# Kernel optimization log

Hardware: AMD Instinct MI355X
Metric: run time of the kernel (lower is better)

Reference implementation:

```python
import jax, jax.numpy as jnp
import numpy as np

T, B, D = 256, 16, 512          # time, batch, intermediate_dim (GRU is seq-first)
HR = 256                         # router_dim
EXPERT_DIMS = [0, 128, 256, 512]
NUM_TASKS = 4
COST_EXP = 1.0
BN_EPS = 1e-5


def _gru(x, w_ih, w_hh, b_ih, b_hh):
    """PyTorch-semantics GRU over axis 0. x: (T, ..., D) -> (T, ..., H).
    Works batched (T,B,D) or unbatched (N,D) exactly like nn.GRU."""
    H = w_hh.shape[1]
    gi = x @ w_ih.T + b_ih            # (T, ..., 3H) input projections, done once
    h0 = jnp.zeros(x.shape[1:-1] + (H,), x.dtype)

    def step(h, gi_t):
        gh = h @ w_hh.T + b_hh
        i_r, i_z, i_n = jnp.split(gi_t, 3, axis=-1)
        h_r, h_z, h_n = jnp.split(gh, 3, axis=-1)
        r = jax.nn.sigmoid(i_r + h_r)
        z = jax.nn.sigmoid(i_z + h_z)
        n = jnp.tanh(i_n + r * h_n)
        h_new = (1.0 - z) * n + z * h
        return h_new, h_new

    _, ys = jax.lax.scan(step, h0, gi)
    return ys


def setup_inputs() -> dict:
    key = jax.random.key(0)
    ks = iter(jax.random.split(key, 64))

    def p(shape, fan_in):
        return (jax.random.normal(next(ks), shape, jnp.float32) / np.sqrt(fan_in)).astype(jnp.float32)

    inp = {
        'x': jax.random.normal(next(ks), (T, B, D), jnp.float32),
        'task_ids': jax.random.randint(next(ks), (T, B), 0, NUM_TASKS),
        # router params
        'router_w_ih': p((3 * HR, D), D),
        'router_w_hh': p((3 * HR, HR), HR),
        'router_b_ih': jnp.zeros((3 * HR,), jnp.float32),
        'router_b_hh': jnp.zeros((3 * HR,), jnp.float32),
        'router_out_w': p((len(EXPERT_DIMS), HR), HR),
        'router_out_b': jnp.zeros((len(EXPERT_DIMS),), jnp.float32),
    }
    for i, H in enumerate(EXPERT_DIMS):
        if H == 0:
            continue
        inp[f'e{i}_w_ih'] = p((3 * H, D), D)
        inp[f'e{i}_w_hh'] = p((3 * H, H), H)
        inp[f'e{i}_b_ih'] = jnp.zeros((3 * H,), jnp.float32)
        inp[f'e{i}_b_hh'] = jnp.zeros((3 * H,), jnp.float32)
        inp[f'e{i}_bn_g'] = jnp.ones((H,), jnp.float32)
        inp[f'e{i}_bn_b'] = jnp.zeros((H,), jnp.float32)
        inp[f'e{i}_out_w'] = p((D, H), H)
        inp[f'e{i}_out_b'] = jnp.zeros((D,), jnp.float32)
    return inp


def reference(x, task_ids,
              router_w_ih, router_w_hh, router_b_ih, router_b_hh,
              router_out_w, router_out_b,
              e1_w_ih, e1_w_hh, e1_b_ih, e1_b_hh, e1_bn_g, e1_bn_b, e1_out_w, e1_out_b,
              e2_w_ih, e2_w_hh, e2_b_ih, e2_b_hh, e2_bn_g, e2_bn_b, e2_out_w, e2_out_b,
              e3_w_ih, e3_w_hh, e3_b_ih, e3_b_hh, e3_bn_g, e3_bn_b, e3_out_w, e3_out_b):
    E = len(EXPERT_DIMS)
    # ---- router: GRU -> ReLU -> Linear -> softmax ----
    hs = _gru(x, router_w_ih, router_w_hh, router_b_ih, router_b_hh)   # (T,B,HR)
    logits = jax.nn.relu(hs) @ router_out_w.T + router_out_b           # (T,B,E)
    raw = jax.nn.softmax(logits, axis=-1)                              # raw_router_output
    # no dropout configured -> router_output == raw, all experts active

    # ---- task expert usage losses ----
    costs = jnp.asarray([d ** COST_EXP for d in EXPERT_DIMS], logits.dtype)
    eul = jnp.einsum('tbe,e->tb', raw, costs).reshape(-1)
    tflat = task_ids.reshape(-1)
    sums = jax.ops.segment_sum(eul, tflat, num_segments=NUM_TASKS)
    cnts = jax.ops.segment_sum(jnp.ones_like(eul), tflat, num_segments=NUM_TASKS)
    task_losses = sums / cnts                                           # (NUM_TASKS,)

    # ---- experts: each sees the flat (N,D) tokens as ONE unbatched GRU sequence ----
    flat_x = x.reshape(-1, D)                                           # (N,D)
    gates = raw.reshape(-1, E)                                          # (N,E)
    out = gates[:, 0:1] * flat_x                                        # expert 0 = identity

    eps = [(e1_w_ih, e1_w_hh, e1_b_ih, e1_b_hh, e1_bn_g, e1_bn_b, e1_out_w, e1_out_b),
           (e2_w_ih, e2_w_hh, e2_b_ih, e2_b_hh, e2_bn_g, e2_bn_b, e2_out_w, e2_out_b),
           (e3_w_ih, e3_w_hh, e3_b_ih, e3_b_hh, e3_bn_g, e3_bn_b, e3_out_w, e3_out_b)]
    for i, (w_ih, w_hh, b_ih, b_hh, g, b, ow, ob) in enumerate(eps, start=1):
        h = _gru(flat_x, w_ih, w_hh, b_ih, b_hh)                        # (N,H) unbatched seq
        mu = h.mean(0)
        var = ((h - mu) ** 2).mean(0)                                   # biased var (train-mode BN)
        hn = (h - mu) / jnp.sqrt(var + BN_EPS) * g + b
        eo = jax.nn.relu(hn) @ ow.T + ob                                # (N,D)
        out = out + gates[:, i:i + 1] * eo

    final_output = out.reshape(T, B, D)
    return final_output, raw, task_losses
```

## Files before the change

### kernel.cpp

```cpp
#include <hip/hip_runtime.h>
#include <math.h>

constexpr int TT = 256, BB = 16, DD = 512;
constexpr int NTOK = 4096;
constexpr int RTOT = 3456;
constexpr int E1OFF = 768, E2OFF = 1152, E3OFF = 1920;

constexpr size_t OFF_TSUM = 0;
constexpr size_t OFF_TCNT = 16;
constexpr size_t OFF_CNT  = 32;
constexpr size_t ZBYTES   = 64;
constexpr size_t OFF_GI   = 4096;
constexpr size_t OFF_HS   = OFF_GI  + (size_t)NTOK*RTOT*4;
constexpr size_t OFF_HA3  = OFF_HS  + (size_t)NTOK*256*4;
constexpr size_t OFF_HA2  = OFF_HA3 + (size_t)NTOK*512*4;
constexpr size_t OFF_HA1  = OFF_HA2 + (size_t)NTOK*256*4;
constexpr size_t OFF_AP   = OFF_HA1 + (size_t)NTOK*128*4;
constexpr size_t OFF_MU   = OFF_AP  + (size_t)NTOK*896*4;
constexpr size_t OFF_RSTD = OFF_MU  + 896*4;
constexpr size_t POISON_BYTES = (size_t)NTOK*(256+512+256+128)*4;

__device__ __forceinline__ bool is_poison(float v) {
  return __float_as_uint(v) == 0xAAAAAAAAu;
}

__device__ __forceinline__ float fast_sigmoid(float x) {
  const float xc = fminf(fmaxf(x, -30.f), 30.f);
  return __fdividef(1.f, 1.f + __expf(-xc));
}
__device__ __forceinline__ float fast_tanh(float x) {
  const float xc = fminf(fmaxf(x, -15.f), 15.f);
  const float e = __expf(-2.f * xc);
  return (1.f - e) * __fdividef(1.f, 1.f + e);
}

__global__ __launch_bounds__(256) void gemm1_kernel(
    const float* __restrict__ X,
    const float* __restrict__ wR, const float* __restrict__ w1,
    const float* __restrict__ w2, const float* __restrict__ w3,
    const float* __restrict__ bR, const float* __restrict__ b1,
    const float* __restrict__ b2, const float* __restrict__ b3,
    float* __restrict__ GI)
{
  __shared__ float At[32*64];
  __shared__ float Bt[32*64];
  const int n0 = blockIdx.x * 64;
  const int r0 = blockIdx.y * 64;
  const float* W; const float* bias; int rs;
  if (r0 < 768)       { W = wR; bias = bR; rs = 0; }
  else if (r0 < 1152) { W = w1; bias = b1; rs = 768; }
  else if (r0 < 1920) { W = w2; bias = b2; rs = 1152; }
  else                { W = w3; bias = b3; rs = 1920; }
  const int lr0 = r0 - rs;
  const int tid = threadIdx.x;
  const int lm = tid & 63, lk4 = tid >> 6;
  const int tx = tid & 15, ty = tid >> 4;
  float acc[4][4];
#pragma unroll
  for (int i = 0; i < 4; ++i)
#pragma unroll
    for (int q = 0; q < 4; ++q) acc[i][q] = 0.f;

  for (int kb = 0; kb < 512; kb += 32) {
    const float4 a0 = *(const float4*)(X + (size_t)(n0+lm)*512 + kb + lk4*8);
    const float4 a1 = *(const float4*)(X + (size_t)(n0+lm)*512 + kb + lk4*8 + 4);
    const float4 c0 = *(const float4*)(W + (size_t)(lr0+lm)*512 + kb + lk4*8);
    const float4 c1 = *(const float4*)(W + (size_t)(lr0+lm)*512 + kb + lk4*8 + 4);
    __syncthreads();
    At[(lk4*8+0)*64+lm]=a0.x; At[(lk4*8+1)*64+lm]=a0.y; At[(lk4*8+2)*64+lm]=a0.z; At[(lk4*8+3)*64+lm]=a0.w;
    At[(lk4*8+4)*64+lm]=a1.x; At[(lk4*8+5)*64+lm]=a1.y; At[(lk4*8+6)*64+lm]=a1.z; At[(lk4*8+7)*64+lm]=a1.w;
    Bt[(lk4*8+0)*64+lm]=c0.x; Bt[(lk4*8+1)*64+lm]=c0.y; Bt[(lk4*8+2)*64+lm]=c0.z; Bt[(lk4*8+3)*64+lm]=c0.w;
    Bt[(lk4*8+4)*64+lm]=c1.x; Bt[(lk4*8+5)*64+lm]=c1.y; Bt[(lk4*8+6)*64+lm]=c1.z; Bt[(lk4*8+7)*64+lm]=c1.w;
    __syncthreads();
#pragma unroll
    for (int k = 0; k < 32; ++k) {
      const float4 av = *(const float4*)&At[k*64 + ty*4];
      const float4 bv = *(const float4*)&Bt[k*64 + tx*4];
      acc[0][0]=fmaf(av.x,bv.x,acc[0][0]); acc[0][1]=fmaf(av.x,bv.y,acc[0][1]); acc[0][2]=fmaf(av.x,bv.z,acc[0][2]); acc[0][3]=fmaf(av.x,bv.w,acc[0][3]);
      acc[1][0]=fmaf(av.y,bv.x,acc[1][0]); acc[1][1]=fmaf(av.y,bv.y,acc[1][1]); acc[1][2]=fmaf(av.y,bv.z,acc[1][2]); acc[1][3]=fmaf(av.y,bv.w,acc[1][3]);
      acc[2][0]=fmaf(av.z,bv.x,acc[2][0]); acc[2][1]=fmaf(av.z,bv.y,acc[2][1]); acc[2][2]=fmaf(av.z,bv.z,acc[2][2]); acc[2][3]=fmaf(av.z,bv.w,acc[2][3]);
      acc[3][0]=fmaf(av.w,bv.x,acc[3][0]); acc[3][1]=fmaf(av.w,bv.y,acc[3][1]); acc[3][2]=fmaf(av.w,bv.z,acc[3][2]); acc[3][3]=fmaf(av.w,bv.w,acc[3][3]);
    }
  }
  const float4 bb = *(const float4*)(bias + lr0 + tx*4);
#pragma unroll
  for (int i = 0; i < 4; ++i) {
    float4 o;
    o.x = acc[i][0] + bb.x; o.y = acc[i][1] + bb.y; o.z = acc[i][2] + bb.z; o.w = acc[i][3] + bb.w;
    *(float4*)(GI + (size_t)(n0+ty*4+i)*RTOT + r0 + tx*4) = o;
  }
}

struct ScanArgs {
  const float* GI;
  const float* rwhh; const float* rbhh; float* hs;
  const float* w1; const float* b1; float* ha1;
  const float* w2; const float* b2; float* ha2;
  const float* w3; const float* b3; float* ha3;
  int* cnt;
};

template<int H, int OPW>
__device__ void expert_scan(const float* __restrict__ GIe, const float* __restrict__ whh,
                            const float* __restrict__ bhh, float* __restrict__ hall,
                            float* __restrict__ sm, int wg)
{
  constexpr int KCN = 512 / OPW;
  constexpr int CHUNK = H / KCN;
  constexpr int NF4 = CHUNK / 4;
  const int tid = threadIdx.x;
  const int j = tid / KCN, kc = tid % KCN;
  const int jg = wg * OPW + j;
  const int lane = tid & 63;

  float4 wr[NF4], wz[NF4], wn[NF4];
#pragma unroll
  for (int i4 = 0; i4 < NF4; ++i4) {
    const int kk = kc * CHUNK + ((i4 + kc) & (NF4 - 1)) * 4;
    wr[i4] = *(const float4*)(whh + (size_t)jg * H + kk);
    wz[i4] = *(const float4*)(whh + (size_t)(H + jg) * H + kk);
    wn[i4] = *(const float4*)(whh + (size_t)(2*H + jg) * H + kk);
  }
  float gbr = 0.f, gbz = 0.f, gbn = 0.f, hprev = 0.f;
  if (kc == 0) { gbr = bhh[jg]; gbz = bhh[H + jg]; gbn = bhh[2*H + jg]; }

  float gAr, gAz, gAn, gBr, gBz, gBn;
  { const float* g = GIe + (size_t)kc * RTOT;
    gAr = g[jg]; gAz = g[H + jg]; gAn = g[2*H + jg]; }
  { const float* g = GIe + (size_t)(KCN + kc) * RTOT;
    gBr = g[jg]; gBz = g[H + jg]; gBn = g[2*H + jg]; }

  for (int t = 0; t < NTOK; ++t) {
    float val = 0.f;
    if (tid < H && t > 0) {
      const volatile float* p = (const volatile float*)(hall + (size_t)(t - 1) * H + tid);
      val = *p;
      while (is_poison(val)) val = *p;
    }
    if (tid < H) sm[(size_t)(t & 1) * H + tid] = val;
    __syncthreads();
    const float* hbuf = sm + (size_t)(t & 1) * H;

    const int m = t & (KCN - 1);
    const int src = (lane & ~(KCN - 1)) | m;
    const float gr0 = __shfl(gAr, src);
    const float gz0 = __shfl(gAz, src);
    const float gn0 = __shfl(gAn, src);

    float pr = 0.f, pz = 0.f, pn = 0.f;
#pragma unroll
    for (int i4 = 0; i4 < NF4; ++i4) {
      const float4 h4 = *(const float4*)(hbuf + kc * CHUNK + ((i4 + kc) & (NF4 - 1)) * 4);
      pr = fmaf(wr[i4].x, h4.x, pr); pr = fmaf(wr[i4].y, h4.y, pr);
      pr = fmaf(wr[i4].z, h4.z, pr); pr = fmaf(wr[i4].w, h4.w, pr);
      pz = fmaf(wz[i4].x, h4.x, pz); pz = fmaf(wz[i4].y, h4.y, pz);
      pz = fmaf(wz[i4].z, h4.z, pz); pz = fmaf(wz[i4].w, h4.w, pz);
      pn = fmaf(wn[i4].x, h4.x, pn); pn = fmaf(wn[i4].y, h4.y, pn);
      pn = fmaf(wn[i4].z, h4.z, pn); pn = fmaf(wn[i4].w, h4.w, pn);
    }
#pragma unroll
    for (int off = KCN / 2; off; off >>= 1) {
      pr += __shfl_down(pr, off); pz += __shfl_down(pz, off); pn += __shfl_down(pn, off);
    }
    if (kc == 0) {
      const float rg = fast_sigmoid(gr0 + gbr + pr);
      const float zg = fast_sigmoid(gz0 + gbz + pz);
      const float nn = fast_tanh(gn0 + rg * (pn + gbn));
      const float hn = (1.f - zg) * nn + zg * hprev;
      hprev = hn;
      *(volatile float*)(hall + (size_t)t * H + jg) = hn;
    }
    if (m == KCN - 1) {
      gAr = gBr; gAz = gBz; gAn = gBn;
      const int nb = t + 1 + KCN;
      if (nb + kc < NTOK) {
        const float* g = GIe + (size_t)(nb + kc) * RTOT;
        gBr = g[jg]; gBz = g[H + jg]; gBn = g[2*H + jg];
      }
    }
  }
}

__device__ void router_scan(const float* __restrict__ GI, const float* __restrict__ whh,
                            const float* __restrict__ bhh, float* __restrict__ hs,
                            float* __restrict__ sm, int wg)
{
  float* hsmB = sm;
  float* pbuf = sm + 16 * 260;
  const int tid = threadIdx.x;
  const int j = tid >> 4, kc = tid & 15;
  const int jg = wg * 32 + j;
  float4 wr4[4], wz4[4], wn4[4];
#pragma unroll
  for (int i4 = 0; i4 < 4; ++i4) {
    const int kk = kc * 16 + ((i4 + kc) & 3) * 4;
    wr4[i4] = *(const float4*)(whh + (size_t)jg * 256 + kk);
    wz4[i4] = *(const float4*)(whh + (size_t)(256 + jg) * 256 + kk);
    wn4[i4] = *(const float4*)(whh + (size_t)(512 + jg) * 256 + kk);
  }
  const int b2 = tid >> 5, j2 = tid & 31;
  const int jg2 = wg * 32 + j2;
  const float gbr = bhh[jg2], gbz = bhh[256 + jg2], gbn = bhh[512 + jg2];
  float gr0, gz0, gn0, gr1, gz1, gn1;
  { const float* g = GI + (size_t)b2 * RTOT;        gr0 = g[jg2]; gz0 = g[256 + jg2]; gn0 = g[512 + jg2]; }
  { const float* g = GI + (size_t)(16 + b2) * RTOT; gr1 = g[jg2]; gz1 = g[256 + jg2]; gn1 = g[512 + jg2]; }
  const int pb = tid >> 5, pk = (tid & 31) * 8;

  for (int t = 0; t < TT; ++t) {
    float gr2 = 0.f, gz2 = 0.f, gn2 = 0.f;
    if (t + 2 < TT) {
      const float* g = GI + (size_t)((t + 2) * 16 + b2) * RTOT;
      gr2 = g[jg2]; gz2 = g[256 + jg2]; gn2 = g[512 + jg2];
    }
    float v[8];
    if (t == 0) {
#pragma unroll
      for (int u = 0; u < 8; ++u) v[u] = 0.f;
    } else {
      const volatile float* q = (const volatile float*)(hs + (size_t)(t - 1) * 4096 + tid * 8);
#pragma unroll
      for (int u = 0; u < 8; ++u) v[u] = q[u];
      bool bad = true;
      while (bad) {
        bad = false;
#pragma unroll
        for (int u = 0; u < 8; ++u)
          if (is_poison(v[u])) { v[u] = q[u]; bad = true; }
      }
    }
    __syncthreads();
    *(float4*)(hsmB + pb * 260 + pk)     = make_float4(v[0], v[1], v[2], v[3]);
    *(float4*)(hsmB + pb * 260 + pk + 4) = make_float4(v[4], v[5], v[6], v[7]);
    __syncthreads();
    float ar[16], az[16], an[16];
#pragma unroll
    for (int b = 0; b < 16; ++b) { ar[b] = 0.f; az[b] = 0.f; an[b] = 0.f; }
#pragma unroll
    for (int i4 = 0; i4 < 4; ++i4) {
      const int col = kc * 16 + ((i4 + kc) & 3) * 4;
#pragma unroll
      for (int b = 0; b < 16; ++b) {
        const float4 h4 = *(const float4*)(hsmB + b * 260 + col);
        ar[b] = fmaf(wr4[i4].x, h4.x, ar[b]); ar[b] = fmaf(wr4[i4].y, h4.y, ar[b]);
        ar[b] = fmaf(wr4[i4].z, h4.z, ar[b]); ar[b] = fmaf(wr4[i4].w, h4.w, ar[b]);
        az[b] = fmaf(wz4[i4].x, h4.x, az[b]); az[b] = fmaf(wz4[i4].y, h4.y, az[b]);
        az[b] = fmaf(wz4[i4].z, h4.z, az[b]); az[b] = fmaf(wz4[i4].w, h4.w, az[b]);
        an[b] = fmaf(wn4[i4].x, h4.x, an[b]); an[b] = fmaf(wn4[i4].y, h4.y, an[b]);
        an[b] = fmaf(wn4[i4].z, h4.z, an[b]); an[b] = fmaf(wn4[i4].w, h4.w, an[b]);
      }
    }
#pragma unroll
    for (int off = 8; off; off >>= 1) {
#pragma unroll
      for (int b = 0; b < 16; ++b) {
        ar[b] += __shfl_down(ar[b], off);
        az[b] += __shfl_down(az[b], off);
        an[b] += __shfl_down(an[b], off);
      }
    }
    if (kc == 0) {
#pragma unroll
      for (int b = 0; b < 16; ++b) {
        pbuf[(b * 32 + j) * 3 + 0] = ar[b];
        pbuf[(b * 32 + j) * 3 + 1] = az[b];
        pbuf[(b * 32 + j) * 3 + 2] = an[b];
      }
    }
    __syncthreads();
    const float pr = pbuf[(b2 * 32 + j2) * 3 + 0];
    const float pz = pbuf[(b2 * 32 + j2) * 3 + 1];
    const float pn = pbuf[(b2 * 32 + j2) * 3 + 2];
    const float hprev = hsmB[b2 * 260 + jg2];
    const float rg = 1.f / (1.f + expf(-(gr0 + gbr + pr)));
    const float zg = 1.f / (1.f + expf(-(gz0 + gbz + pz)));
    const float nn = tanhf(gn0 + rg * (pn + gbn));
    const float hn = (1.f - zg) * nn + zg * hprev;
    *(volatile float*)(hs + (size_t)t * 4096 + b2 * 256 + jg2) = hn;
    gr0 = gr1; gz0 = gz1; gn0 = gn1;
    gr1 = gr2; gz1 = gz2; gn1 = gn2;
  }
}

__global__ __launch_bounds__(512, 1) void scan_kernel(ScanArgs A)
{
  __shared__ __attribute__((aligned(16))) float sm[16 * 260 + 1536];
  __shared__ int role_s[2];
  if (threadIdx.x == 0) {
    unsigned x;
    asm volatile("s_getreg_b32 %0, hwreg(HW_REG_XCC_ID)" : "=s"(x));
    const int xcd = (int)(x & 7u);
    role_s[0] = xcd;
    role_s[1] = atomicAdd(A.cnt + xcd, 1);
  }
  __syncthreads();
  const int xcd = role_s[0], r = role_s[1];
  if (xcd == 0)      { if (r < 32) expert_scan<512, 16>(A.GI + E3OFF, A.w3, A.b3, A.ha3, sm, r); }
  else if (xcd == 1) { if (r < 8)  router_scan(A.GI, A.rwhh, A.rbhh, A.hs, sm, r); }
  else if (xcd == 2) { if (r < 8)  expert_scan<256, 32>(A.GI + E2OFF, A.w2, A.b2, A.ha2, sm, r); }
  else if (xcd == 3) { if (r < 4)  expert_scan<128, 32>(A.GI + E1OFF, A.w1, A.b1, A.ha1, sm, r); }
}

__global__ __launch_bounds__(256) void router_out_kernel(
    const float* __restrict__ hs, const float* __restrict__ ow, const float* __restrict__ ob,
    const int* __restrict__ tids, float* __restrict__ raw_out,
    float* __restrict__ tsum, float* __restrict__ tcnt)
{
  const int tid = threadIdx.x;
  const int lane = tid & 63, w = tid >> 6;
  const int n = blockIdx.x * 4 + w;
  float s0 = 0.f, s1 = 0.f, s2 = 0.f, s3 = 0.f;
#pragma unroll
  for (int q = 0; q < 4; ++q) {
    const int jj = lane + q * 64;
    float h = hs[(size_t)n * 256 + jj];
    h = h > 0.f ? h : 0.f;
    s0 = fmaf(h, ow[jj], s0);
    s1 = fmaf(h, ow[256 + jj], s1);
    s2 = fmaf(h, ow[512 + jj], s2);
    s3 = fmaf(h, ow[768 + jj], s3);
  }
  for (int off = 32; off; off >>= 1) {
    s0 += __shfl_xor(s0, off); s1 += __shfl_xor(s1, off);
    s2 += __shfl_xor(s2, off); s3 += __shfl_xor(s3, off);
  }
  if (lane == 0) {
    const float l0 = s0 + ob[0], l1 = s1 + ob[1], l2 = s2 + ob[2], l3 = s3 + ob[3];
    const float m = fmaxf(fmaxf(l0, l1), fmaxf(l2, l3));
    const float e0 = expf(l0 - m), e1 = expf(l1 - m), e2 = expf(l2 - m), e3 = expf(l3 - m);
    const float inv = 1.f / (e0 + e1 + e2 + e3);
    float4 rv; rv.x = e0 * inv; rv.y = e1 * inv; rv.z = e2 * inv; rv.w = e3 * inv;
    *(float4*)(raw_out + (size_t)n * 4) = rv;
    const float eul = rv.y * 128.f + rv.z * 256.f + rv.w * 512.f;
    const int tk = tids[n];
    atomicAdd(&tsum[tk], eul);
    atomicAdd(&tcnt[tk], 1.f);
  }
}

__global__ __launch_bounds__(256) void bn_stats_kernel(
    const float* __restrict__ h1, const float* __restrict__ h2, const float* __restrict__ h3,
    float* __restrict__ mu, float* __restrict__ rstd)
{
  const int c = blockIdx.x;
  const float* hp; int He, hc;
  if (c < 128)      { hp = h1; He = 128; hc = c; }
  else if (c < 384) { hp = h2; He = 256; hc = c - 128; }
  else              { hp = h3; He = 512; hc = c - 384; }
  float s = 0.f, s2 = 0.f;
  for (int r = threadIdx.x; r < NTOK; r += 256) {
    const float v = hp[(size_t)r * He + hc];
    s += v; s2 = fmaf(v, v, s2);
  }
  for (int off = 32; off; off >>= 1) { s += __shfl_xor(s, off); s2 += __shfl_xor(s2, off); }
  __shared__ float red[8];
  const int lane = threadIdx.x & 63, w = threadIdx.x >> 6;
  if (lane == 0) { red[w] = s; red[4 + w] = s2; }
  __syncthreads();
  if (threadIdx.x == 0) {
    const float S = red[0] + red[1] + red[2] + red[3];
    const float S2 = red[4] + red[5] + red[6] + red[7];
    const float m = S * (1.f / 4096.f);
    float v = S2 * (1.f / 4096.f) - m * m;
    v = v > 0.f ? v : 0.f;
    mu[c] = m;
    rstd[c] = 1.f / sqrtf(v + 1e-5f);
  }
}

__global__ __launch_bounds__(256) void aprime_kernel(
    const float* __restrict__ h1, const float* __restrict__ h2, const float* __restrict__ h3,
    const float* __restrict__ g1, const float* __restrict__ be1,
    const float* __restrict__ g2, const float* __restrict__ be2,
    const float* __restrict__ g3, const float* __restrict__ be3,
    const float* __restrict__ mu, const float* __restrict__ rstd,
    const float* __restrict__ raw, float* __restrict__ Ap,
    const float* __restrict__ tsum, const float* __restrict__ tcnt, float* __restrict__ tl_out)
{
  if (blockIdx.x == 4096) {
    if (threadIdx.x < 4) tl_out[threadIdx.x] = tsum[threadIdx.x] / tcnt[threadIdx.x];
    return;
  }
  const int n = blockIdx.x;
  for (int c = threadIdx.x; c < 896; c += 256) {
    const float* hp; const float* gg; const float* bb; int He, hc, e;
    if (c < 128)      { hp = h1; gg = g1; bb = be1; He = 128; hc = c;       e = 1; }
    else if (c < 384) { hp = h2; gg = g2; bb = be2; He = 256; hc = c - 128; e = 2; }
    else              { hp = h3; gg = g3; bb = be3; He = 512; hc = c - 384; e = 3; }
    const float h = hp[(size_t)n * He + hc];
    float v = (h - mu[c]) * rstd[c] * gg[hc] + bb[hc];
    v = v > 0.f ? v : 0.f;
    Ap[(size_t)n * 896 + c] = raw[(size_t)n * 4 + e] * v;
  }
}

__global__ __launch_bounds__(256) void out_gemm_kernel(
    const float* __restrict__ Ap,
    const float* __restrict__ ow1, const float* __restrict__ ow2, const float* __restrict__ ow3,
    const float* __restrict__ ob1, const float* __restrict__ ob2, const float* __restrict__ ob3,
    const float* __restrict__ X, const float* __restrict__ raw, float* __restrict__ out)
{
  __shared__ float At[32*64];
  __shared__ float Bt[32*64];
  const int n0 = blockIdx.x * 64;
  const int d0 = blockIdx.y * 64;
  const int tid = threadIdx.x;
  const int lm = tid & 63, lk4 = tid >> 6;
  const int tx = tid & 15, ty = tid >> 4;
  float acc[4][4];
#pragma unroll
  for (int i = 0; i < 4; ++i)
#pragma unroll
    for (int q = 0; q < 4; ++q) acc[i][q] = 0.f;

  for (int kb = 0; kb < 896; kb += 32) {
    const float* W; int He, ko;
    if (kb < 128)      { W = ow1; He = 128; ko = 0; }
    else if (kb < 384) { W = ow2; He = 256; ko = 128; }
    else               { W = ow3; He = 512; ko = 384; }
    const float4 a0 = *(const float4*)(Ap + (size_t)(n0+lm)*896 + kb + lk4*8);
    const float4 a1 = *(const float4*)(Ap + (size_t)(n0+lm)*896 + kb + lk4*8 + 4);
    const float4 c0 = *(const float4*)(W + (size_t)(d0+lm)*He + (kb - ko) + lk4*8);
    const float4 c1 = *(const float4*)(W + (size_t)(d0+lm)*He + (kb - ko) + lk4*8 + 4);
    __syncthreads();
    At[(lk4*8+0)*64+lm]=a0.x; At[(lk4*8+1)*64+lm]=a0.y; At[(lk4*8+2)*64+lm]=a0.z; At[(lk4*8+3)*64+lm]=a0.w;
    At[(lk4*8+4)*64+lm]=a1.x; At[(lk4*8+5)*64+lm]=a1.y; At[(lk4*8+6)*64+lm]=a1.z; At[(lk4*8+7)*64+lm]=a1.w;
    Bt[(lk4*8+0)*64+lm]=c0.x; Bt[(lk4*8+1)*64+lm]=c0.y; Bt[(lk4*8+2)*64+lm]=c0.z; Bt[(lk4*8+3)*64+lm]=c0.w;
    Bt[(lk4*8+4)*64+lm]=c1.x; Bt[(lk4*8+5)*64+lm]=c1.y; Bt[(lk4*8+6)*64+lm]=c1.z; Bt[(lk4*8+7)*64+lm]=c1.w;
    __syncthreads();
#pragma unroll
    for (int k = 0; k < 32; ++k) {
      const float4 av = *(const float4*)&At[k*64 + ty*4];
      const float4 bv = *(const float4*)&Bt[k*64 + tx*4];
      acc[0][0]=fmaf(av.x,bv.x,acc[0][0]); acc[0][1]=fmaf(av.x,bv.y,acc[0][1]); acc[0][2]=fmaf(av.x,bv.z,acc[0][2]); acc[0][3]=fmaf(av.x,bv.w,acc[0][3]);
      acc[1][0]=fmaf(av.y,bv.x,acc[1][0]); acc[1][1]=fmaf(av.y,bv.y,acc[1][1]); acc[1][2]=fmaf(av.y,bv.z,acc[1][2]); acc[1][3]=fmaf(av.y,bv.w,acc[1][3]);
      acc[2][0]=fmaf(av.z,bv.x,acc[2][0]); acc[2][1]=fmaf(av.z,bv.y,acc[2][1]); acc[2][2]=fmaf(av.z,bv.z,acc[2][2]); acc[2][3]=fmaf(av.z,bv.w,acc[2][3]);
      acc[3][0]=fmaf(av.w,bv.x,acc[3][0]); acc[3][1]=fmaf(av.w,bv.y,acc[3][1]); acc[3][2]=fmaf(av.w,bv.z,acc[3][2]); acc[3][3]=fmaf(av.w,bv.w,acc[3][3]);
    }
  }
#pragma unroll
  for (int i = 0; i < 4; ++i) {
    const int n = n0 + ty * 4 + i;
    const float4 g  = *(const float4*)(raw + (size_t)n * 4);
    const float4 xv = *(const float4*)(X + (size_t)n * 512 + d0 + tx * 4);
    const float4 o1 = *(const float4*)(ob1 + d0 + tx * 4);
    const float4 o2 = *(const float4*)(ob2 + d0 + tx * 4);
    const float4 o3 = *(const float4*)(ob3 + d0 + tx * 4);
    float4 o;
    o.x = acc[i][0] + g.x*xv.x + g.y*o1.x + g.z*o2.x + g.w*o3.x;
    o.y = acc[i][1] + g.x*xv.y + g.y*o1.y + g.z*o2.y + g.w*o3.y;
    o.z = acc[i][2] + g.x*xv.z + g.y*o1.z + g.z*o2.z + g.w*o3.z;
    o.w = acc[i][3] + g.x*xv.w + g.y*o1.w + g.z*o2.w + g.w*o3.w;
    *(float4*)(out + (size_t)n * 512 + d0 + tx * 4) = o;
  }
}

extern "C" void kernel_launch(void* const* d_in, const int* in_sizes, int n_in,
                              void* d_out, int out_size, void* d_ws, size_t ws_size,
                              hipStream_t stream) {
  const float* x    = (const float*)d_in[0];
  const int*   tids = (const int*)d_in[1];
  const float* rwih = (const float*)d_in[2];
  const float* rwhh = (const float*)d_in[3];
  const float* rbih = (const float*)d_in[4];
  const float* rbhh = (const float*)d_in[5];
  const float* row  = (const float*)d_in[6];
  const float* rob  = (const float*)d_in[7];
  const float* w1ih = (const float*)d_in[8];
  const float* w1hh = (const float*)d_in[9];
  const float* b1ih = (const float*)d_in[10];
  const float* b1hh = (const float*)d_in[11];
  const float* bn1g = (const float*)d_in[12];
  const float* bn1b = (const float*)d_in[13];
  const float* ow1  = (const float*)d_in[14];
  const float* ob1  = (const float*)d_in[15];
  const float* w2ih = (const float*)d_in[16];
  const float* w2hh = (const float*)d_in[17];
  const float* b2ih = (const float*)d_in[18];
  const float* b2hh = (const float*)d_in[19];
  const float* bn2g = (const float*)d_in[20];
  const float* bn2b = (const float*)d_in[21];
  const float* ow2  = (const float*)d_in[22];
  const float* ob2  = (const float*)d_in[23];
  const float* w3ih = (const float*)d_in[24];
  const float* w3hh = (const float*)d_in[25];
  const float* b3ih = (const float*)d_in[26];
  const float* b3hh = (const float*)d_in[27];
  const float* bn3g = (const float*)d_in[28];
  const float* bn3b = (const float*)d_in[29];
  const float* ow3  = (const float*)d_in[30];
  const float* ob3  = (const float*)d_in[31];

  char* ws = (char*)d_ws;
  float* tsum = (float*)(ws + OFF_TSUM);
  float* tcnt = (float*)(ws + OFF_TCNT);
  int*   cnt  = (int*)(ws + OFF_CNT);
  float* GI   = (float*)(ws + OFF_GI);
  float* hs   = (float*)(ws + OFF_HS);
  float* ha3  = (float*)(ws + OFF_HA3);
  float* ha2  = (float*)(ws + OFF_HA2);
  float* ha1  = (float*)(ws + OFF_HA1);
  float* Ap   = (float*)(ws + OFF_AP);
  float* mu   = (float*)(ws + OFF_MU);
  float* rstd = (float*)(ws + OFF_RSTD);

  float* outp = (float*)d_out;
  float* rawp = outp + (size_t)NTOK * DD;
  float* tlp  = rawp + (size_t)NTOK * 4;

  hipMemsetAsync(ws, 0, ZBYTES, stream);
  hipMemsetAsync(ws + OFF_HS, 0xAA, POISON_BYTES, stream);

  gemm1_kernel<<<dim3(64, 54), 256, 0, stream>>>(x, rwih, w1ih, w2ih, w3ih,
                                                 rbih, b1ih, b2ih, b3ih, GI);

  ScanArgs sa;
  sa.GI = GI; sa.rwhh = rwhh; sa.rbhh = rbhh; sa.hs = hs;
  sa.w1 = w1hh; sa.b1 = b1hh; sa.ha1 = ha1;
  sa.w2 = w2hh; sa.b2 = b2hh; sa.ha2 = ha2;
  sa.w3 = w3hh; sa.b3 = b3hh; sa.ha3 = ha3;
  sa.cnt = cnt;
  scan_kernel<<<dim3(320), dim3(512), 0, stream>>>(sa);

  router_out_kernel<<<dim3(1024), 256, 0, stream>>>(hs, row, rob, tids, rawp, tsum, tcnt);
  bn_stats_kernel<<<dim3(896), 256, 0, stream>>>(ha1, ha2, ha3, mu, rstd);
  aprime_kernel<<<dim3(4097), 256, 0, stream>>>(ha1, ha2, ha3, bn1g, bn1b, bn2g, bn2b,
                                                bn3g, bn3b, mu, rstd, rawp, Ap,
                                                tsum, tcnt, tlp);

  out_gemm_kernel<<<dim3(64, 8), 256, 0, stream>>>(Ap, ow1, ow2, ow3, ob1, ob2, ob3,
                                                   x, rawp, outp);
}
```

Before: 6.400 ms.

## Move expert-1 GRU scan to a single-block kernel and add cache-prefetch warps

The 128-wide expert-1 recurrence moves out of the multi-block polling scan into its own single 1024-thread block. There the hidden state is exchanged through shared memory with one barrier per step, instead of poison-polled global memory across four blocks. The combined scan kernel grows to 576 threads per block. The extra 64 threads in the expert scans touch hidden-state rows two steps ahead, to warm the cache for the polling loads. Because the new kernel is launched on the same stream before the combined scan, its 4096 serial steps no longer overlap with the other scans, which risks lengthening the critical path.

```diff
diff --git a/kernel.cpp b/kernel.cpp
--- a/kernel.cpp
+++ b/kernel.cpp
@@ -91,62 +91,61 @@
   }
 }
 
-struct ScanArgs {
-  const float* GI;
-  const float* rwhh; const float* rbhh; float* hs;
-  const float* w1; const float* b1; float* ha1;
-  const float* w2; const float* b2; float* ha2;
-  const float* w3; const float* b3; float* ha3;
-  int* cnt;
-};
-
-template<int H, int OPW>
-__device__ void expert_scan(const float* __restrict__ GIe, const float* __restrict__ whh,
-                            const float* __restrict__ bhh, float* __restrict__ hall,
-                            float* __restrict__ sm, int wg)
-{
-  constexpr int KCN = 512 / OPW;
-  constexpr int CHUNK = H / KCN;
-  constexpr int NF4 = CHUNK / 4;
+__global__ __launch_bounds__(1024, 1) void e1_scan_kernel(
+    const float* __restrict__ GIe, const float* __restrict__ whh,
+    const float* __restrict__ bhh, float* __restrict__ hall)
+{
+  constexpr int H = 128, CHUNK = 16, NF4 = 4;
+  __shared__ __attribute__((aligned(16))) float sm[2 * H];
   const int tid = threadIdx.x;
-  const int j = tid / KCN, kc = tid % KCN;
-  const int jg = wg * OPW + j;
   const int lane = tid & 63;
+  const int j = tid >> 3;
+  const int kc = tid & 7;
 
   float4 wr[NF4], wz[NF4], wn[NF4];
 #pragma unroll
   for (int i4 = 0; i4 < NF4; ++i4) {
     const int kk = kc * CHUNK + ((i4 + kc) & (NF4 - 1)) * 4;
-    wr[i4] = *(const float4*)(whh + (size_t)jg * H + kk);
-    wz[i4] = *(const float4*)(whh + (size_t)(H + jg) * H + kk);
-    wn[i4] = *(const float4*)(whh + (size_t)(2*H + jg) * H + kk);
+    wr[i4] = *(const float4*)(whh + (size_t)j * H + kk);
+    wz[i4] = *(const float4*)(whh + (size_t)(H + j) * H + kk);
+    wn[i4] = *(const float4*)(whh + (size_t)(2*H + j) * H + kk);
   }
   float gbr = 0.f, gbz = 0.f, gbn = 0.f, hprev = 0.f;
-  if (kc == 0) { gbr = bhh[jg]; gbz = bhh[H + jg]; gbn = bhh[2*H + jg]; }
-
-  float gAr, gAz, gAn, gBr, gBz, gBn;
-  { const float* g = GIe + (size_t)kc * RTOT;
-    gAr = g[jg]; gAz = g[H + jg]; gAn = g[2*H + jg]; }
-  { const float* g = GIe + (size_t)(KCN + kc) * RTOT;
-    gBr = g[jg]; gBz = g[H + jg]; gBn = g[2*H + jg]; }
+  if (kc == 0) { gbr = bhh[j]; gbz = bhh[H + j]; gbn = bhh[2*H + j]; }
+
+  float gA0r, gA0z, gA0n, gA1r, gA1z, gA1n;
+  float gB0r, gB0z, gB0n, gB1r, gB1z, gB1n;
+  { const float* g = GIe + (size_t)kc * RTOT;       gA0r=g[j]; gA0z=g[H+j]; gA0n=g[2*H+j]; }
+  { const float* g = GIe + (size_t)(8+kc) * RTOT;   gA1r=g[j]; gA1z=g[H+j]; gA1n=g[2*H+j]; }
+  { const float* g = GIe + (size_t)(16+kc) * RTOT;  gB0r=g[j]; gB0z=g[H+j]; gB0n=g[2*H+j]; }
+  { const float* g = GIe + (size_t)(24+kc) * RTOT;  gB1r=g[j]; gB1z=g[H+j]; gB1n=g[2*H+j]; }
+
+  if (tid < H) sm[tid] = 0.f;
+  __syncthreads();
 
   for (int t = 0; t < NTOK; ++t) {
-    float val = 0.f;
-    if (tid < H && t > 0) {
-      const volatile float* p = (const volatile float*)(hall + (size_t)(t - 1) * H + tid);
-      val = *p;
-      while (is_poison(val)) val = *p;
-    }
-    if (tid < H) sm[(size_t)(t & 1) * H + tid] = val;
-    __syncthreads();
+    if ((t & 15) == 0 && t > 0) {
+      gA0r=gB0r; gA0z=gB0z; gA0n=gB0n; gA1r=gB1r; gA1z=gB1z; gA1n=gB1n;
+      const int nb = t + 16;
+      if (nb + kc < NTOK) {
+        const float* g0 = GIe + (size_t)(nb + kc) * RTOT;
+        gB0r=g0[j]; gB0z=g0[H+j]; gB0n=g0[2*H+j];
+      }
+      if (nb + 8 + kc < NTOK) {
+        const float* g1 = GIe + (size_t)(nb + 8 + kc) * RTOT;
+        gB1r=g1[j]; gB1z=g1[H+j]; gB1n=g1[2*H+j];
+      }
+    }
+    const int hi = (t >> 3) & 1;
+    const float sr = hi ? gA1r : gA0r;
+    const float sz = hi ? gA1z : gA0z;
+    const float sn = hi ? gA1n : gA0n;
+    const int src = (lane & ~7) | (t & 7);
+    const float gr0 = __shfl(sr, src);
+    const float gz0 = __shfl(sz, src);
+    const float gn0 = __shfl(sn, src);
+
     const float* hbuf = sm + (size_t)(t & 1) * H;
-
-    const int m = t & (KCN - 1);
-    const int src = (lane & ~(KCN - 1)) | m;
-    const float gr0 = __shfl(gAr, src);
-    const float gz0 = __shfl(gAz, src);
-    const float gn0 = __shfl(gAn, src);
-
     float pr = 0.f, pz = 0.f, pn = 0.f;
 #pragma unroll
     for (int i4 = 0; i4 < NF4; ++i4) {
@@ -158,25 +157,124 @@
       pn = fmaf(wn[i4].x, h4.x, pn); pn = fmaf(wn[i4].y, h4.y, pn);
       pn = fmaf(wn[i4].z, h4.z, pn); pn = fmaf(wn[i4].w, h4.w, pn);
     }
-#pragma unroll
-    for (int off = KCN / 2; off; off >>= 1) {
-      pr += __shfl_down(pr, off); pz += __shfl_down(pz, off); pn += __shfl_down(pn, off);
-    }
+    pr += __shfl_down(pr, 4); pz += __shfl_down(pz, 4); pn += __shfl_down(pn, 4);
+    pr += __shfl_down(pr, 2); pz += __shfl_down(pz, 2); pn += __shfl_down(pn, 2);
+    pr += __shfl_down(pr, 1); pz += __shfl_down(pz, 1); pn += __shfl_down(pn, 1);
     if (kc == 0) {
       const float rg = fast_sigmoid(gr0 + gbr + pr);
       const float zg = fast_sigmoid(gz0 + gbz + pz);
       const float nn = fast_tanh(gn0 + rg * (pn + gbn));
       const float hn = (1.f - zg) * nn + zg * hprev;
       hprev = hn;
-      *(volatile float*)(hall + (size_t)t * H + jg) = hn;
-    }
-    if (m == KCN - 1) {
-      gAr = gBr; gAz = gBz; gAn = gBn;
-      const int nb = t + 1 + KCN;
-      if (nb + kc < NTOK) {
-        const float* g = GIe + (size_t)(nb + kc) * RTOT;
-        gBr = g[jg]; gBz = g[H + jg]; gBn = g[2*H + jg];
-      }
+      sm[(size_t)((t + 1) & 1) * H + j] = hn;
+      hall[(size_t)t * H + j] = hn;
+    }
+    __syncthreads();
+  }
+}
+
+struct ScanArgs {
+  const float* GI;
+  const float* rwhh; const float* rbhh; float* hs;
+  const float* w2; const float* b2; float* ha2;
+  const float* w3; const float* b3; float* ha3;
+  int* cnt;
+};
+
+template<int H, int OPW>
+__device__ void expert_scan(const float* __restrict__ GIe, const float* __restrict__ whh,
+                            const float* __restrict__ bhh, float* __restrict__ hall,
+                            float* __restrict__ sm, int wg)
+{
+  constexpr int KCN = 512 / OPW;
+  constexpr int CHUNK = H / KCN;
+  constexpr int NF4 = CHUNK / 4;
+  constexpr int PSTR = H / 64;
+  const int tid = threadIdx.x;
+  const bool act = (tid < 512);
+  const int lane = tid & 63;
+  const int j = (tid / KCN) & (OPW - 1);
+  const int kc = tid & (KCN - 1);
+  const int jg = wg * OPW + j;
+
+  float4 wr[NF4], wz[NF4], wn[NF4];
+  float gbr = 0.f, gbz = 0.f, gbn = 0.f, hprev = 0.f;
+  float gAr = 0.f, gAz = 0.f, gAn = 0.f, gBr = 0.f, gBz = 0.f, gBn = 0.f;
+  if (act) {
+#pragma unroll
+    for (int i4 = 0; i4 < NF4; ++i4) {
+      const int kk = kc * CHUNK + ((i4 + kc) & (NF4 - 1)) * 4;
+      wr[i4] = *(const float4*)(whh + (size_t)jg * H + kk);
+      wz[i4] = *(const float4*)(whh + (size_t)(H + jg) * H + kk);
+      wn[i4] = *(const float4*)(whh + (size_t)(2*H + jg) * H + kk);
+    }
+    if (kc == 0) { gbr = bhh[jg]; gbz = bhh[H + jg]; gbn = bhh[2*H + jg]; }
+    { const float* g = GIe + (size_t)kc * RTOT;
+      gAr = g[jg]; gAz = g[H + jg]; gAn = g[2*H + jg]; }
+    { const float* g = GIe + (size_t)(KCN + kc) * RTOT;
+      gBr = g[jg]; gBz = g[H + jg]; gBn = g[2*H + jg]; }
+  } else {
+    const int l = tid - 512;
+    volatile const float* p0 = (volatile const float*)(hall + (size_t)0 * H + l * PSTR);
+    volatile const float* p1 = (volatile const float*)(hall + (size_t)1 * H + l * PSTR);
+    float d0 = *p0, d1 = *p1;
+    asm volatile("" :: "v"(d0), "v"(d1));
+  }
+
+  for (int t = 0; t < NTOK; ++t) {
+    if (act) {
+      float val = 0.f;
+      if (tid < H && t > 0) {
+        const volatile float* p = (const volatile float*)(hall + (size_t)(t - 1) * H + tid);
+        val = *p;
+        while (is_poison(val)) val = *p;
+      }
+      if (tid < H) sm[(size_t)(t & 1) * H + tid] = val;
+    }
+    __syncthreads();
+    if (act) {
+      const int m = t & (KCN - 1);
+      if (m == 0 && t > 0) {
+        gAr = gBr; gAz = gBz; gAn = gBn;
+        const int nb = t + KCN;
+        if (nb + kc < NTOK) {
+          const float* g = GIe + (size_t)(nb + kc) * RTOT;
+          gBr = g[jg]; gBz = g[H + jg]; gBn = g[2*H + jg];
+        }
+      }
+      const int src = (lane & ~(KCN - 1)) | m;
+      const float gr0 = __shfl(gAr, src);
+      const float gz0 = __shfl(gAz, src);
+      const float gn0 = __shfl(gAn, src);
+      const float* hbuf = sm + (size_t)(t & 1) * H;
+      float pr = 0.f, pz = 0.f, pn = 0.f;
+#pragma unroll
+      for (int i4 = 0; i4 < NF4; ++i4) {
+        const float4 h4 = *(const float4*)(hbuf + kc * CHUNK + ((i4 + kc) & (NF4 - 1)) * 4);
+        pr = fmaf(wr[i4].x, h4.x, pr); pr = fmaf(wr[i4].y, h4.y, pr);
+        pr = fmaf(wr[i4].z, h4.z, pr); pr = fmaf(wr[i4].w, h4.w, pr);
+        pz = fmaf(wz[i4].x, h4.x, pz); pz = fmaf(wz[i4].y, h4.y, pz);
+        pz = fmaf(wz[i4].z, h4.z, pz); pz = fmaf(wz[i4].w, h4.w, pz);
+        pn = fmaf(wn[i4].x, h4.x, pn); pn = fmaf(wn[i4].y, h4.y, pn);
+        pn = fmaf(wn[i4].w, h4.w, pn); pn = fmaf(wn[i4].z, h4.z, pn);
+      }
+#pragma unroll
+      for (int off = KCN / 2; off; off >>= 1) {
+        pr += __shfl_down(pr, off); pz += __shfl_down(pz, off); pn += __shfl_down(pn, off);
+      }
+      if (kc == 0) {
+        const float rg = fast_sigmoid(gr0 + gbr + pr);
+        const float zg = fast_sigmoid(gz0 + gbz + pz);
+        const float nn = fast_tanh(gn0 + rg * (pn + gbn));
+        const float hn = (1.f - zg) * nn + zg * hprev;
+        hprev = hn;
+        *(volatile float*)(hall + (size_t)t * H + jg) = hn;
+      }
+    } else if (t + 2 < NTOK) {
+      const int l = tid - 512;
+      volatile const float* p = (volatile const float*)(hall + (size_t)(t + 2) * H + l * PSTR);
+      float d = *p;
+      asm volatile("" :: "v"(d));
     }
   }
 }
@@ -188,100 +286,114 @@
   float* hsmB = sm;
   float* pbuf = sm + 16 * 260;
   const int tid = threadIdx.x;
-  const int j = tid >> 4, kc = tid & 15;
+  const bool act = (tid < 512);
+  const int j = (tid >> 4) & 31, kc = tid & 15;
   const int jg = wg * 32 + j;
   float4 wr4[4], wz4[4], wn4[4];
-#pragma unroll
-  for (int i4 = 0; i4 < 4; ++i4) {
-    const int kk = kc * 16 + ((i4 + kc) & 3) * 4;
-    wr4[i4] = *(const float4*)(whh + (size_t)jg * 256 + kk);
-    wz4[i4] = *(const float4*)(whh + (size_t)(256 + jg) * 256 + kk);
-    wn4[i4] = *(const float4*)(whh + (size_t)(512 + jg) * 256 + kk);
-  }
-  const int b2 = tid >> 5, j2 = tid & 31;
+  if (act) {
+#pragma unroll
+    for (int i4 = 0; i4 < 4; ++i4) {
+      const int kk = kc * 16 + ((i4 + kc) & 3) * 4;
+      wr4[i4] = *(const float4*)(whh + (size_t)jg * 256 + kk);
+      wz4[i4] = *(const float4*)(whh + (size_t)(256 + jg) * 256 + kk);
+      wn4[i4] = *(const float4*)(whh + (size_t)(512 + jg) * 256 + kk);
+    }
+  }
+  const int b2 = (tid >> 5) & 15, j2 = tid & 31;
   const int jg2 = wg * 32 + j2;
-  const float gbr = bhh[jg2], gbz = bhh[256 + jg2], gbn = bhh[512 + jg2];
-  float gr0, gz0, gn0, gr1, gz1, gn1;
-  { const float* g = GI + (size_t)b2 * RTOT;        gr0 = g[jg2]; gz0 = g[256 + jg2]; gn0 = g[512 + jg2]; }
-  { const float* g = GI + (size_t)(16 + b2) * RTOT; gr1 = g[jg2]; gz1 = g[256 + jg2]; gn1 = g[512 + jg2]; }
-  const int pb = tid >> 5, pk = (tid & 31) * 8;
+  float gbr = 0.f, gbz = 0.f, gbn = 0.f;
+  float gr0 = 0.f, gz0 = 0.f, gn0 = 0.f, gr1 = 0.f, gz1 = 0.f, gn1 = 0.f;
+  if (act) {
+    gbr = bhh[jg2]; gbz = bhh[256 + jg2]; gbn = bhh[512 + jg2];
+    { const float* g = GI + (size_t)b2 * RTOT;        gr0 = g[jg2]; gz0 = g[256 + jg2]; gn0 = g[512 + jg2]; }
+    { const float* g = GI + (size_t)(16 + b2) * RTOT; gr1 = g[jg2]; gz1 = g[256 + jg2]; gn1 = g[512 + jg2]; }
+  }
+  const int pb = (tid >> 5) & 15, pk = (tid & 31) * 8;
 
   for (int t = 0; t < TT; ++t) {
+    float v[8];
+    if (act) {
+      if (t == 0) {
+#pragma unroll
+        for (int u = 0; u < 8; ++u) v[u] = 0.f;
+      } else {
+        const volatile float* q = (const volatile float*)(hs + (size_t)(t - 1) * 4096 + tid * 8);
+#pragma unroll
+        for (int u = 0; u < 8; ++u) v[u] = q[u];
+        bool bad = true;
+        while (bad) {
+          bad = false;
+#pragma unroll
+          for (int u = 0; u < 8; ++u)
+            if (is_poison(v[u])) { v[u] = q[u]; bad = true; }
+        }
+      }
+    }
     float gr2 = 0.f, gz2 = 0.f, gn2 = 0.f;
-    if (t + 2 < TT) {
+    if (act && t + 2 < TT) {
       const float* g = GI + (size_t)((t + 2) * 16 + b2) * RTOT;
       gr2 = g[jg2]; gz2 = g[256 + jg2]; gn2 = g[512 + jg2];
     }
-    float v[8];
-    if (t == 0) {
-#pragma unroll
-      for (int u = 0; u < 8; ++u) v[u] = 0.f;
-    } else {
-      const volatile float* q = (const volatile float*)(hs + (size_t)(t - 1) * 4096 + tid * 8);
-#pragma unroll
-      for (int u = 0; u < 8; ++u) v[u] = q[u];
-      bool bad = true;
-      while (bad) {
-        bad = false;
-#pragma unroll
-        for (int u = 0; u < 8; ++u)
-          if (is_poison(v[u])) { v[u] = q[u]; bad = true; }
-      }
-    }
-    __syncthreads();
-    *(float4*)(hsmB + pb * 260 + pk)     = make_float4(v[0], v[1], v[2], v[3]);
-    *(float4*)(hsmB + pb * 260 + pk + 4) = make_float4(v[4], v[5], v[6], v[7]);
-    __syncthreads();
-    float ar[16], az[16], an[16];
-#pragma unroll
-    for (int b = 0; b < 16; ++b) { ar[b] = 0.f; az[b] = 0.f; an[b] = 0.f; }
-#pragma unroll
-    for (int i4 = 0; i4 < 4; ++i4) {
-      const int col = kc * 16 + ((i4 + kc) & 3) * 4;
-#pragma unroll
-      for (int b = 0; b < 16; ++b) {
-        const float4 h4 = *(const float4*)(hsmB + b * 260 + col);
-        ar[b] = fmaf(wr4[i4].x, h4.x, ar[b]); ar[b] = fmaf(wr4[i4].y, h4.y, ar[b]);
-        ar[b] = fmaf(wr4[i4].z, h4.z, ar[b]); ar[b] = fmaf(wr4[i4].w, h4.w, ar[b]);
-        az[b] = fmaf(wz4[i4].x, h4.x, az[b]); az[b] = fmaf(wz4[i4].y, h4.y, az[b]);
-        az[b] = fmaf(wz4[i4].z, h4.z, az[b]); az[b] = fmaf(wz4[i4].w, h4.w, az[b]);
-        an[b] = fmaf(wn4[i4].x, h4.x, an[b]); an[b] = fmaf(wn4[i4].y, h4.y, an[b]);
-        an[b] = fmaf(wn4[i4].z, h4.z, an[b]); an[b] = fmaf(wn4[i4].w, h4.w, an[b]);
-      }
-    }
-#pragma unroll
-    for (int off = 8; off; off >>= 1) {
-#pragma unroll
-      for (int b = 0; b < 16; ++b) {
-        ar[b] += __shfl_down(ar[b], off);
-        az[b] += __shfl_down(az[b], off);
-        an[b] += __shfl_down(an[b], off);
-      }
-    }
-    if (kc == 0) {
-#pragma unroll
-      for (int b = 0; b < 16; ++b) {
-        pbuf[(b * 32 + j) * 3 + 0] = ar[b];
-        pbuf[(b * 32 + j) * 3 + 1] = az[b];
-        pbuf[(b * 32 + j) * 3 + 2] = an[b];
-      }
-    }
-    __syncthreads();
-    const float pr = pbuf[(b2 * 32 + j2) * 3 + 0];
-    const float pz = pbuf[(b2 * 32 + j2) * 3 + 1];
-    const float pn = pbuf[(b2 * 32 + j2) * 3 + 2];
-    const float hprev = hsmB[b2 * 260 + jg2];
-    const float rg = 1.f / (1.f + expf(-(gr0 + gbr + pr)));
-    const float zg = 1.f / (1.f + expf(-(gz0 + gbz + pz)));
-    const float nn = tanhf(gn0 + rg * (pn + gbn));
-    const float hn = (1.f - zg) * nn + zg * hprev;
-    *(volatile float*)(hs + (size_t)t * 4096 + b2 * 256 + jg2) = hn;
-    gr0 = gr1; gz0 = gz1; gn0 = gn1;
-    gr1 = gr2; gz1 = gz2; gn1 = gn2;
-  }
-}
-
-__global__ __launch_bounds__(512, 1) void scan_kernel(ScanArgs A)
+    __syncthreads();
+    if (act) {
+      *(float4*)(hsmB + pb * 260 + pk)     = make_float4(v[0], v[1], v[2], v[3]);
+      *(float4*)(hsmB + pb * 260 + pk + 4) = make_float4(v[4], v[5], v[6], v[7]);
+    }
+    __syncthreads();
+    if (act) {
+      float ar[16], az[16], an[16];
+#pragma unroll
+      for (int b = 0; b < 16; ++b) { ar[b] = 0.f; az[b] = 0.f; an[b] = 0.f; }
+#pragma unroll
+      for (int i4 = 0; i4 < 4; ++i4) {
+        const int col = kc * 16 + ((i4 + kc) & 3) * 4;
+#pragma unroll
+        for (int b = 0; b < 16; ++b) {
+          const float4 h4 = *(const float4*)(hsmB + b * 260 + col);
+          ar[b] = fmaf(wr4[i4].x, h4.x, ar[b]); ar[b] = fmaf(wr4[i4].y, h4.y, ar[b]);
+          ar[b] = fmaf(wr4[i4].z, h4.z, ar[b]); ar[b] = fmaf(wr4[i4].w, h4.w, ar[b]);
+          az[b] = fmaf(wz4[i4].x, h4.x, az[b]); az[b] = fmaf(wz4[i4].y, h4.y, az[b]);
+          az[b] = fmaf(wz4[i4].z, h4.z, az[b]); az[b] = fmaf(wz4[i4].w, h4.w, az[b]);
+          an[b] = fmaf(wn4[i4].x, h4.x, an[b]); an[b] = fmaf(wn4[i4].y, h4.y, an[b]);
+          an[b] = fmaf(wn4[i4].z, h4.z, an[b]); an[b] = fmaf(wn4[i4].w, h4.w, an[b]);
+        }
+      }
+#pragma unroll
+      for (int off = 8; off; off >>= 1) {
+#pragma unroll
+        for (int b = 0; b < 16; ++b) {
+          ar[b] += __shfl_down(ar[b], off);
+          az[b] += __shfl_down(az[b], off);
+          an[b] += __shfl_down(an[b], off);
+        }
+      }
+      if (kc == 0) {
+#pragma unroll
+        for (int b = 0; b < 16; ++b) {
+          pbuf[(b * 32 + j) * 3 + 0] = ar[b];
+          pbuf[(b * 32 + j) * 3 + 1] = az[b];
+          pbuf[(b * 32 + j) * 3 + 2] = an[b];
+        }
+      }
+    }
+    __syncthreads();
+    if (act) {
+      const float pr = pbuf[(b2 * 32 + j2) * 3 + 0];
+      const float pz = pbuf[(b2 * 32 + j2) * 3 + 1];
+      const float pn = pbuf[(b2 * 32 + j2) * 3 + 2];
+      const float hprev = hsmB[b2 * 260 + jg2];
+      const float rg = 1.f / (1.f + expf(-(gr0 + gbr + pr)));
+      const float zg = 1.f / (1.f + expf(-(gz0 + gbz + pz)));
+      const float nn = tanhf(gn0 + rg * (pn + gbn));
+      const float hn = (1.f - zg) * nn + zg * hprev;
+      *(volatile float*)(hs + (size_t)t * 4096 + b2 * 256 + jg2) = hn;
+      gr0 = gr1; gz0 = gz1; gn0 = gn1;
+      gr1 = gr2; gz1 = gz2; gn1 = gn2;
+    }
+  }
+}
+
+__global__ __launch_bounds__(576, 1) void scan_kernel(ScanArgs A)
 {
   __shared__ __attribute__((aligned(16))) float sm[16 * 260 + 1536];
   __shared__ int role_s[2];
@@ -297,7 +409,6 @@
   if (xcd == 0)      { if (r < 32) expert_scan<512, 16>(A.GI + E3OFF, A.w3, A.b3, A.ha3, sm, r); }
   else if (xcd == 1) { if (r < 8)  router_scan(A.GI, A.rwhh, A.rbhh, A.hs, sm, r); }
   else if (xcd == 2) { if (r < 8)  expert_scan<256, 32>(A.GI + E2OFF, A.w2, A.b2, A.ha2, sm, r); }
-  else if (xcd == 3) { if (r < 4)  expert_scan<128, 32>(A.GI + E1OFF, A.w1, A.b1, A.ha1, sm, r); }
 }
 
 __global__ __launch_bounds__(256) void router_out_kernel(
@@ -513,13 +624,14 @@
   gemm1_kernel<<<dim3(64, 54), 256, 0, stream>>>(x, rwih, w1ih, w2ih, w3ih,
                                                  rbih, b1ih, b2ih, b3ih, GI);
 
+  e1_scan_kernel<<<dim3(1), dim3(1024), 0, stream>>>(GI + E1OFF, w1hh, b1hh, ha1);
+
   ScanArgs sa;
   sa.GI = GI; sa.rwhh = rwhh; sa.rbhh = rbhh; sa.hs = hs;
-  sa.w1 = w1hh; sa.b1 = b1hh; sa.ha1 = ha1;
   sa.w2 = w2hh; sa.b2 = b2hh; sa.ha2 = ha2;
   sa.w3 = w3hh; sa.b3 = b3hh; sa.ha3 = ha3;
   sa.cnt = cnt;
-  scan_kernel<<<dim3(320), dim3(512), 0, stream>>>(sa);
+  scan_kernel<<<dim3(320), dim3(576), 0, stream>>>(sa);
 
   router_out_kernel<<<dim3(1024), 256, 0, stream>>>(hs, row, rob, tids, rawp, tsum, tcnt);
   bn_stats_kernel<<<dim3(896), 256, 0, stream>>>(ha1, ha2, ha3, mu, rstd);
```

Result: slower. 11.04 ms (+72.4%).

## Run expert GRU scans on four active waves with more workgroups

Applied to the files above, without the earlier changes.

Adds a variant of the expert recurrent scan where only 256 threads (four wavefronts) do the matvec. Each thread polls two hidden values when H is 512, while the idle waves just match the barriers. The 512-dim expert keeps 32 workgroups at 16 outputs each. The 256-dim expert now spreads across 16 workgroups of 16 outputs instead of 8 of 32. The input-gate prefetch rotation moves to the start of each step, and one FMA pair is reordered. The aim is cheaper per-step barrier and reduction latency on the serial recurrence, at the cost of more cross-workgroup polling traffic and more registers per active thread.

```diff
diff --git a/kernel.cpp b/kernel.cpp
--- a/kernel.cpp
+++ b/kernel.cpp
@@ -101,6 +101,98 @@
 };
 
 template<int H, int OPW>
+__device__ void expert_scan4w(const float* __restrict__ GIe, const float* __restrict__ whh,
+                              const float* __restrict__ bhh, float* __restrict__ hall,
+                              float* __restrict__ sm, int wg)
+{
+  constexpr int ACT = 256;
+  constexpr int KCN = ACT / OPW;
+  constexpr int C   = H / KCN;
+  constexpr int NF4 = C / 4;
+  constexpr int PP  = H / ACT;
+  const int tid = threadIdx.x;
+  if (tid >= ACT) {
+    for (int t = 0; t < NTOK; ++t) __syncthreads();
+    return;
+  }
+  const int j = tid / KCN, kc = tid % KCN;
+  const int jg = wg * OPW + j;
+  const int lane = tid & 63;
+
+  float4 wr[NF4], wz[NF4], wn[NF4];
+#pragma unroll
+  for (int i4 = 0; i4 < NF4; ++i4) {
+    const int kk = kc * C + ((i4 + kc) & (NF4 - 1)) * 4;
+    wr[i4] = *(const float4*)(whh + (size_t)jg * H + kk);
+    wz[i4] = *(const float4*)(whh + (size_t)(H + jg) * H + kk);
+    wn[i4] = *(const float4*)(whh + (size_t)(2*H + jg) * H + kk);
+  }
+  float gbr = 0.f, gbz = 0.f, gbn = 0.f, hprev = 0.f;
+  if (kc == 0) { gbr = bhh[jg]; gbz = bhh[H + jg]; gbn = bhh[2*H + jg]; }
+
+  float gAr, gAz, gAn, gBr, gBz, gBn;
+  { const float* g = GIe + (size_t)kc * RTOT;
+    gAr = g[jg]; gAz = g[H + jg]; gAn = g[2*H + jg]; }
+  { const float* g = GIe + (size_t)(KCN + kc) * RTOT;
+    gBr = g[jg]; gBz = g[H + jg]; gBn = g[2*H + jg]; }
+
+  for (int t = 0; t < NTOK; ++t) {
+    float v0 = 0.f, v1 = 0.f;
+    if (t > 0) {
+      const volatile float* p = (const volatile float*)(hall + (size_t)(t - 1) * H + tid * PP);
+      v0 = p[0];
+      while (is_poison(v0)) v0 = p[0];
+      if constexpr (PP == 2) {
+        v1 = p[1];
+        while (is_poison(v1)) v1 = p[1];
+      }
+    }
+    sm[(size_t)(t & 1) * H + tid * PP] = v0;
+    if constexpr (PP == 2) sm[(size_t)(t & 1) * H + tid * PP + 1] = v1;
+    __syncthreads();
+    const float* hbuf = sm + (size_t)(t & 1) * H;
+
+    const int m = t & (KCN - 1);
+    if (m == 0 && t > 0) {
+      gAr = gBr; gAz = gBz; gAn = gBn;
+      const int nb = t + KCN;
+      if (nb + kc < NTOK) {
+        const float* g = GIe + (size_t)(nb + kc) * RTOT;
+        gBr = g[jg]; gBz = g[H + jg]; gBn = g[2*H + jg];
+      }
+    }
+    const int src = (lane & ~(KCN - 1)) | m;
+    const float gr0 = __shfl(gAr, src);
+    const float gz0 = __shfl(gAz, src);
+    const float gn0 = __shfl(gAn, src);
+
+    float pr = 0.f, pz = 0.f, pn = 0.f;
+#pragma unroll
+    for (int i4 = 0; i4 < NF4; ++i4) {
+      const float4 h4 = *(const float4*)(hbuf + kc * C + ((i4 + kc) & (NF4 - 1)) * 4);
+      pr = fmaf(wr[i4].x, h4.x, pr); pr = fmaf(wr[i4].y, h4.y, pr);
+      pr = fmaf(wr[i4].z, h4.z, pr); pr = fmaf(wr[i4].w, h4.w, pr);
+      pz = fmaf(wz[i4].x, h4.x, pz); pz = fmaf(wz[i4].y, h4.y, pz);
+      pz = fmaf(wz[i4].z, h4.z, pz); pz = fmaf(wz[i4].w, h4.w, pz);
+      pn = fmaf(wn[i4].x, h4.x, pn); pn = fmaf(wn[i4].y, h4.y, pn);
+      pn = fmaf(wn[i4].z, h4.z, pn); pn = fmaf(wn[i4].w, h4.w, pn);
+    }
+#pragma unroll
+    for (int off = KCN / 2; off; off >>= 1) {
+      pr += __shfl_down(pr, off); pz += __shfl_down(pz, off); pn += __shfl_down(pn, off);
+    }
+    if (kc == 0) {
+      const float rg = fast_sigmoid(gr0 + gbr + pr);
+      const float zg = fast_sigmoid(gz0 + gbz + pz);
+      const float nn = fast_tanh(gn0 + rg * (pn + gbn));
+      const float hn = (1.f - zg) * nn + zg * hprev;
+      hprev = hn;
+      *(volatile float*)(hall + (size_t)t * H + jg) = hn;
+    }
+  }
+}
+
+template<int H, int OPW>
 __device__ void expert_scan(const float* __restrict__ GIe, const float* __restrict__ whh,
                             const float* __restrict__ bhh, float* __restrict__ hall,
                             float* __restrict__ sm, int wg)
@@ -142,6 +234,14 @@
     const float* hbuf = sm + (size_t)(t & 1) * H;
 
     const int m = t & (KCN - 1);
+    if (m == 0 && t > 0) {
+      gAr = gBr; gAz = gBz; gAn = gBn;
+      const int nb = t + KCN;
+      if (nb + kc < NTOK) {
+        const float* g = GIe + (size_t)(nb + kc) * RTOT;
+        gBr = g[jg]; gBz = g[H + jg]; gBn = g[2*H + jg];
+      }
+    }
     const int src = (lane & ~(KCN - 1)) | m;
     const float gr0 = __shfl(gAr, src);
     const float gz0 = __shfl(gAz, src);
@@ -156,7 +256,7 @@
       pz = fmaf(wz[i4].x, h4.x, pz); pz = fmaf(wz[i4].y, h4.y, pz);
       pz = fmaf(wz[i4].z, h4.z, pz); pz = fmaf(wz[i4].w, h4.w, pz);
       pn = fmaf(wn[i4].x, h4.x, pn); pn = fmaf(wn[i4].y, h4.y, pn);
-      pn = fmaf(wn[i4].z, h4.z, pn); pn = fmaf(wn[i4].w, h4.w, pn);
+      pn = fmaf(wn[i4].w, h4.w, pn); pn = fmaf(wn[i4].z, h4.z, pn);
     }
 #pragma unroll
     for (int off = KCN / 2; off; off >>= 1) {
@@ -169,14 +269,6 @@
       const float hn = (1.f - zg) * nn + zg * hprev;
       hprev = hn;
       *(volatile float*)(hall + (size_t)t * H + jg) = hn;
-    }
-    if (m == KCN - 1) {
-      gAr = gBr; gAz = gBz; gAn = gBn;
-      const int nb = t + 1 + KCN;
-      if (nb + kc < NTOK) {
-        const float* g = GIe + (size_t)(nb + kc) * RTOT;
-        gBr = g[jg]; gBz = g[H + jg]; gBn = g[2*H + jg];
-      }
     }
   }
 }
@@ -294,9 +386,9 @@
   }
   __syncthreads();
   const int xcd = role_s[0], r = role_s[1];
-  if (xcd == 0)      { if (r < 32) expert_scan<512, 16>(A.GI + E3OFF, A.w3, A.b3, A.ha3, sm, r); }
+  if (xcd == 0)      { if (r < 32) expert_scan4w<512, 16>(A.GI + E3OFF, A.w3, A.b3, A.ha3, sm, r); }
   else if (xcd == 1) { if (r < 8)  router_scan(A.GI, A.rwhh, A.rbhh, A.hs, sm, r); }
-  else if (xcd == 2) { if (r < 8)  expert_scan<256, 32>(A.GI + E2OFF, A.w2, A.b2, A.ha2, sm, r); }
+  else if (xcd == 2) { if (r < 16) expert_scan4w<256, 16>(A.GI + E2OFF, A.w2, A.b2, A.ha2, sm, r); }
   else if (xcd == 3) { if (r < 4)  expert_scan<128, 32>(A.GI + E1OFF, A.w1, A.b1, A.ha1, sm, r); }
 }
 
```

Measured after the change: 6.665 ms. 4.1% more time.
